# Optimization experiments

Measured on AMD Instinct MI355X. Metric: run time of the kernel, lower is better.

The kernel has to match this reference:

```python
import jax, jax.numpy as jnp
import numpy as np

DIM = 768
HEADS = 12
HEAD_DIM = DIM // HEADS
RANK = 8
SCALING = 1.0 / RANK  # lora_alpha / r
SCALE = HEAD_DIM ** -0.5


def setup_inputs() -> dict:
    key = jax.random.key(0)
    ks = jax.random.split(key, 14)
    B, N, D, r = 4, 1024, DIM, RANK
    s = lambda k, shape, sd=0.02: jax.random.normal(k, shape, jnp.float32) * sd
    return {
        "x": jax.random.normal(ks[0], (B, N, D), jnp.float32),
        "qkv_w": s(ks[1], (3 * D, D)),
        "qkv_b": s(ks[2], (3 * D,)),
        "q_base_w": s(ks[3], (D, D)),
        "q_base_b": s(ks[4], (D,)),
        "q_A": s(ks[5], (r, D), 1.0 / r),
        "q_B": s(ks[6], (D, r)),
        "k_base_w": s(ks[7], (D, D)),
        "k_base_b": s(ks[8], (D,)),
        "k_A": s(ks[9], (r, D), 1.0 / r),
        "k_B": s(ks[10], (D, r)),
        "proj_w": s(ks[11], (D, D)),
        "proj_b": s(ks[12], (D,)),
    }


def _lora_linear(x, w, b, A, Bm):
    # base linear + LoRA delta: x@w.T + b + (x@A.T)@B.T * scaling
    return x @ w.T + b + ((x @ A.T) @ Bm.T) * SCALING


def reference(x, qkv_w, qkv_b, q_base_w, q_base_b, q_A, q_B,
              k_base_w, k_base_b, k_A, k_B, proj_w, proj_b):
    B, N, D = x.shape
    H, hd = HEADS, HEAD_DIM
    qkv = (x @ qkv_w.T + qkv_b).reshape(B, N, 3, H, hd).transpose(2, 0, 3, 1, 4)
    q, k, v = qkv[0], qkv[1], qkv[2]  # [B,H,N,hd]
    q_delta = _lora_linear(x, q_base_w, q_base_b, q_A, q_B).reshape(B, N, H, hd).transpose(0, 2, 1, 3)
    k_delta = _lora_linear(x, k_base_w, k_base_b, k_A, k_B).reshape(B, N, H, hd).transpose(0, 2, 1, 3)
    q = q + q_delta
    k = k + k_delta
    attn = jnp.einsum('bhnd,bhmd->bhnm', q, k) * SCALE
    attn = jax.nn.softmax(attn, axis=-1)
    out = jnp.einsum('bhnm,bhmd->bhnd', attn, v)
    out = out.transpose(0, 2, 1, 3).reshape(B, N, D)
    return out @ proj_w.T + proj_b
```

## Files before the change

### kernel.cpp

```cpp
#include <hip/hip_runtime.h>
#include <hip/hip_bf16.h>


typedef _Float16 half8 __attribute__((ext_vector_type(8)));
typedef float f32x4 __attribute__((ext_vector_type(4)));

typedef __attribute__((address_space(3))) unsigned int lds_u32;
typedef __attribute__((address_space(1))) const unsigned int glob_u32;

__device__ __forceinline__ void glds16(const void* g, void* l) {
    __builtin_amdgcn_global_load_lds((glob_u32*)g, (lds_u32*)l, 16, 0, 0);
}

__device__ __forceinline__ float pk2f16(float a, float b) {
    return __builtin_bit_cast(float, __builtin_amdgcn_cvt_pkrtz(a, b));
}

#define SMSCALE 0.18033688011112042f

constexpr size_t OFF_WX = 0;
constexpr size_t OFF_PH = OFF_WX + (size_t)2304*800*2;
constexpr size_t OFF_XE = OFF_PH + (size_t)768*768*2;
constexpr size_t OFF_QH = OFF_XE + (size_t)4096*800*2;
constexpr size_t OFF_KH = OFF_QH + (size_t)48*1024*64*2;
constexpr size_t OFF_VT = OFF_KH + (size_t)48*1024*64*2;
constexpr size_t OFF_AO = OFF_VT + (size_t)48*1024*64*2;

__global__ __launch_bounds__(256)
void prep(const float* __restrict__ qkv_w, const float* __restrict__ qkv_b,
          const float* __restrict__ qw, const float* __restrict__ qbias,
          const float* __restrict__ kw, const float* __restrict__ kbias,
          const float* __restrict__ proj_w, const float* __restrict__ qB,
          const float* __restrict__ kB,
          _Float16* __restrict__ Wx, _Float16* __restrict__ Ph) {
    const int t = threadIdx.x, bb = blockIdx.x;
    if (bb < 2304) {
        const int n = bb;
        const float rs = (n < 768) ? SMSCALE : 1.0f;
        const float* wsrc = qkv_w + (size_t)n * 768;
        const float* fold = (n < 768) ? (qw + (size_t)n * 768)
                          : (n < 1536 ? (kw + (size_t)(n - 768) * 768) : nullptr);
        _Float16* dst = Wx + (size_t)n * 800;
#pragma unroll
        for (int i = 0; i < 3; ++i) {
            const int c = t + i * 256;
            float v = wsrc[c];
            if (fold) v += fold[c];
            dst[c] = (_Float16)(v * rs);
        }
        if (t < 32) {
            float v = 0.f;
            if (t < 8)       { if (n < 768) v = rs * 0.125f * qB[n * 8 + t]; }
            else if (t < 16) { if (n >= 768 && n < 1536) v = 0.125f * kB[(size_t)(n - 768) * 8 + (t - 8)]; }
            else if (t == 16) v = rs * (qkv_b[n] + (n < 768 ? qbias[n] : (n < 1536 ? kbias[n - 768] : 0.f)));
            dst[768 + t] = (_Float16)v;
        }
    } else {
        const size_t idx = ((size_t)(bb - 2304) * 256 + t) * 4;
        const float4 v = *(const float4*)(proj_w + idx);
        _Float16* d = Ph + idx;
        d[0] = (_Float16)v.x; d[1] = (_Float16)v.y;
        d[2] = (_Float16)v.z; d[3] = (_Float16)v.w;
    }
}

__global__ __launch_bounds__(256)
void lora_xa(const float* __restrict__ x, const float* __restrict__ qA,
             const float* __restrict__ kA, _Float16* __restrict__ Xe) {
    __shared__ float As_[16][772];
    __shared__ float xs[8][768];
    const int t = threadIdx.x, m0 = blockIdx.x * 8;

#pragma unroll
    for (int i = t * 4; i < 12288; i += 1024) {
        const int r = i / 768, c = i - r * 768;
        const float4 v = *(const float4*)((r < 8 ? qA + (size_t)r * 768 : kA + (size_t)(r - 8) * 768) + c);
        As_[r][c] = v.x; As_[r][c + 1] = v.y; As_[r][c + 2] = v.z; As_[r][c + 3] = v.w;
    }
#pragma unroll
    for (int i = t * 4; i < 6144; i += 1024) {
        const int r = i / 768, c = i - r * 768;
        const float4 v = *(const float4*)(x + (size_t)(m0 + r) * 768 + c);
        xs[r][c] = v.x; xs[r][c + 1] = v.y; xs[r][c + 2] = v.z; xs[r][c + 3] = v.w;
        _Float16* d = Xe + (size_t)(m0 + r) * 800 + c;
        d[0] = (_Float16)v.x; d[1] = (_Float16)v.y; d[2] = (_Float16)v.z; d[3] = (_Float16)v.w;
    }
    __syncthreads();

    const int j = t >> 4, lane = t & 15;
#pragma unroll
    for (int r = 0; r < 8; ++r) {
        float acc = 0.f;
        for (int k = lane; k < 768; k += 16) acc += xs[r][k] * As_[j][k];
        acc += __shfl_xor(acc, 1); acc += __shfl_xor(acc, 2);
        acc += __shfl_xor(acc, 4); acc += __shfl_xor(acc, 8);
        if (lane == 0) Xe[(size_t)(m0 + r) * 800 + 768 + j] = (_Float16)acc;
    }
    if (t < 128) {
        const int r = t >> 4, c = t & 15;
        Xe[(size_t)(m0 + r) * 800 + 784 + c] = (c == 0) ? (_Float16)1.f : (_Float16)0.f;
    }
}

template<int BM, int BN, int MODE>
__global__ __launch_bounds__(256)
void gemm_h(const _Float16* __restrict__ A, const _Float16* __restrict__ Bw,
            const int lda, const int ldb, const int nsteps,
            const float* __restrict__ bias,
            _Float16* __restrict__ Oq, _Float16* __restrict__ Ok, _Float16* __restrict__ Ov,
            float* __restrict__ Co) {
    constexpr int CA = BM / 16, CB = BN / 16, CT = CA + CB;
    constexpr int MI = BM / 32, NI = BN / 32;
    __shared__ __align__(16) _Float16 As[2][BM * 32];
    __shared__ __align__(16) _Float16 Bs[2][BN * 32];
    const int t = threadIdx.x;
    const int w = t >> 6, l = t & 63;
    const int l15 = l & 15, lg = l >> 4;
    const int wm = w >> 1, wn = w & 1;

    const int gx = gridDim.x;
    int lin = blockIdx.y * gx + blockIdx.x;
    lin = (lin & 7) * ((gx * gridDim.y) >> 3) + (lin >> 3);
    const int n0 = (lin % gx) * BN, m0 = (lin / gx) * BM;

    const _Float16* Abase = A + (size_t)(m0 + l15) * lda + lg * 8;
    const _Float16* Bbase = Bw + (size_t)(n0 + l15) * ldb + lg * 8;

    f32x4 acc[MI][NI];
#pragma unroll
    for (int mi = 0; mi < MI; ++mi)
#pragma unroll
        for (int ni = 0; ni < NI; ++ni) acc[mi][ni] = 0.f;

#pragma unroll
    for (int c = w; c < CT; c += 4) {
        if (c < CA) glds16(Abase + (size_t)(c * 16) * lda, &As[0][c * 512]);
        else        glds16(Bbase + (size_t)((c - CA) * 16) * ldb, &Bs[0][(c - CA) * 512]);
    }
    __syncthreads();

    for (int s = 0; s < nsteps; ++s) {
        const int cur = s & 1;
        if (s + 1 < nsteps) {
            const int ko = (s + 1) * 32;
#pragma unroll
            for (int c = w; c < CT; c += 4) {
                if (c < CA) glds16(Abase + (size_t)(c * 16) * lda + ko, &As[cur ^ 1][c * 512]);
                else        glds16(Bbase + (size_t)((c - CA) * 16) * ldb + ko, &Bs[cur ^ 1][(c - CA) * 512]);
            }
        }
        half8 a[MI], b[NI];
#pragma unroll
        for (int mi = 0; mi < MI; ++mi) a[mi] = *(const half8*)&As[cur][(wm * MI + mi) * 512 + l * 8];
#pragma unroll
        for (int ni = 0; ni < NI; ++ni) b[ni] = *(const half8*)&Bs[cur][(wn * NI + ni) * 512 + l * 8];
#pragma unroll
        for (int mi = 0; mi < MI; ++mi)
#pragma unroll
            for (int ni = 0; ni < NI; ++ni)
                acc[mi][ni] = __builtin_amdgcn_mfma_f32_16x16x32_f16(a[mi], b[ni], acc[mi][ni], 0, 0, 0);
        __syncthreads();
    }

    if (MODE == 0) {
        const int sel = (n0 >= 1536) ? 2 : (n0 >= 768 ? 1 : 0);
        const int b_ = m0 >> 10, nnb = m0 & 1023;
        if (sel < 2) {
            _Float16* dst = (sel == 0) ? Oq : Ok;
            const int jb = n0 - sel * 768;
#pragma unroll
            for (int mi = 0; mi < MI; ++mi)
#pragma unroll
                for (int reg = 0; reg < 4; ++reg) {
                    const int nn = nnb + wm * (BM / 2) + mi * 16 + lg * 4 + reg;
#pragma unroll
                    for (int ni = 0; ni < NI; ++ni) {
                        const int jj = jb + wn * (BN / 2) + ni * 16 + l15;
                        const int h = jj >> 6, d = jj & 63;
                        dst[(((size_t)(b_ * 12 + h)) * 1024 + nn) * 64 + d] = (_Float16)acc[mi][ni][reg];
                    }
                }
        } else {
#pragma unroll
            for (int mi = 0; mi < MI; ++mi) {
                const int nn = nnb + wm * (BM / 2) + mi * 16 + lg * 4;
#pragma unroll
                for (int ni = 0; ni < NI; ++ni) {
                    const int jj = (n0 - 1536) + wn * (BN / 2) + ni * 16 + l15;
                    const int h = jj >> 6, d = jj & 63;
                    float2 pv;
                    pv.x = pk2f16(acc[mi][ni][0], acc[mi][ni][1]);
                    pv.y = pk2f16(acc[mi][ni][2], acc[mi][ni][3]);
                    *(float2*)&Ov[(((size_t)(b_ * 12 + h)) * 64 + d) * 1024 + nn] = pv;
                }
            }
        }
    } else {
#pragma unroll
        for (int mi = 0; mi < MI; ++mi)
#pragma unroll
            for (int reg = 0; reg < 4; ++reg) {
                const int m = m0 + wm * (BM / 2) + mi * 16 + lg * 4 + reg;
#pragma unroll
                for (int ni = 0; ni < NI; ++ni) {
                    const int n = n0 + wn * (BN / 2) + ni * 16 + l15;
                    Co[(size_t)m * 768 + n] = acc[mi][ni][reg] + bias[n];
                }
            }
    }
}

#define STAGEK(kbt, buf) { \
_Pragma("unroll") \
    for (int i = 0; i < 4; ++i) { \
        const int c = w * 4 + i; \
        glds16(Kp + (size_t)((kbt) * 64 + (c >> 1) * 16 + l15) * 64 + (c & 1) * 32 + lg * 8, &Ks[buf][c * 512]); \
    } }
#define STAGEV(kbt, buf) { \
_Pragma("unroll") \
    for (int i = 0; i < 4; ++i) { \
        const int c = w * 4 + i; \
        glds16(Vp + (size_t)((c >> 1) * 16 + l15) * 1024 + (kbt) * 64 + (c & 1) * 32 + lg * 8, &Vs[buf][c * 512]); \
    } }
#define QK(buf, s) { \
    half8 kreg[8]; \
_Pragma("unroll") \
    for (int c = 0; c < 8; ++c) kreg[c] = *(const half8*)&Ks[buf][c * 512 + l * 8]; \
_Pragma("unroll") \
    for (int mi = 0; mi < 2; ++mi) \
_Pragma("unroll") \
        for (int nj = 0; nj < 4; ++nj) { \
            s[mi][nj] = 0.f; \
_Pragma("unroll") \
            for (int kh = 0; kh < 2; ++kh) \
                s[mi][nj] = __builtin_amdgcn_mfma_f32_16x16x32_f16(kreg[nj * 2 + kh], qf[mi][kh], s[mi][nj], 0, 0, 0); \
        } }
#define EXPP(ph, s) { \
_Pragma("unroll") \
    for (int mi = 0; mi < 2; ++mi) { \
        float ls = 0.f; \
_Pragma("unroll") \
        for (int nj = 0; nj < 4; ++nj) { \
            const float p0 = __builtin_amdgcn_exp2f(s[mi][nj][0]); \
            const float p1 = __builtin_amdgcn_exp2f(s[mi][nj][1]); \
            const float p2 = __builtin_amdgcn_exp2f(s[mi][nj][2]); \
            const float p3 = __builtin_amdgcn_exp2f(s[mi][nj][3]); \
            ls += (p0 + p1) + (p2 + p3); \
            float2 pk; \
            pk.x = pk2f16(p0, p1); \
            pk.y = pk2f16(p2, p3); \
            const int off = (mi * 2 + (nj >> 1)) * 512 + (2 * (nj & 1) + (lg >> 1)) * 128 \
                          + l15 * 8 + 4 * (lg & 1); \
            *(float2*)&Ps[w][ph][off] = pk; \
        } \
        lsum[mi] += ls; \
    } }
#define PV(ph, buf) { \
    half8 pf[2][2]; \
_Pragma("unroll") \
    for (int mi = 0; mi < 2; ++mi) \
_Pragma("unroll") \
        for (int kh = 0; kh < 2; ++kh) \
            pf[mi][kh] = *(const half8*)&Ps[w][ph][(mi * 2 + kh) * 512 + l * 8]; \
_Pragma("unroll") \
    for (int fj = 0; fj < 4; ++fj) \
_Pragma("unroll") \
        for (int kh = 0; kh < 2; ++kh) { \
            const half8 vf = *(const half8*)&Vs[buf][(fj * 2 + kh) * 512 + l * 8]; \
_Pragma("unroll") \
            for (int mi = 0; mi < 2; ++mi) \
                o[mi][fj] = __builtin_amdgcn_mfma_f32_16x16x32_f16(pf[mi][kh], vf, o[mi][fj], 0, 0, 0); \
        } }

__global__ __launch_bounds__(128)
void attn5(const _Float16* __restrict__ Q, const _Float16* __restrict__ K,
           const _Float16* __restrict__ Vt, _Float16* __restrict__ AO) {
    __shared__ __align__(16) _Float16 Ks[2][4096];
    __shared__ __align__(16) _Float16 Vs[2][4096];
    __shared__ __align__(16) _Float16 Ps[2][2][2048];
    __shared__ float sums[2][32];
    const int t = threadIdx.x;
    const int w = t >> 6, l = t & 63;
    const int l15 = l & 15, lg = l >> 4;

    int lin = blockIdx.y * 16 + blockIdx.x;
    lin = (lin & 7) * 96 + (lin >> 3);
    const int qb = lin & 15, bh = lin >> 4;

    const _Float16* Qp = Q  + (size_t)bh * 65536;
    const _Float16* Kp = K  + (size_t)bh * 65536;
    const _Float16* Vp = Vt + (size_t)bh * 65536;

    STAGEK(0, 0); STAGEK(1, 1); STAGEV(0, 0);
    half8 qf[2][2];
#pragma unroll
    for (int mi = 0; mi < 2; ++mi)
#pragma unroll
        for (int kh = 0; kh < 2; ++kh)
            qf[mi][kh] = *(const half8*)&Qp[(size_t)(qb * 64 + w * 32 + mi * 16 + l15) * 64 + kh * 32 + lg * 8];

    f32x4 o[2][4];
#pragma unroll
    for (int mi = 0; mi < 2; ++mi)
#pragma unroll
        for (int fj = 0; fj < 4; ++fj) o[mi][fj] = 0.f;
    float lsum[2] = {0.f, 0.f};
    __syncthreads();

    {
        f32x4 s[2][4];
        QK(0, s);
        EXPP(0, s);
    }
    __syncthreads();

    for (int kb = 0; kb < 15; ++kb) {
        const int cb = kb & 1, nb = cb ^ 1;
        if (kb + 2 < 16) STAGEK(kb + 2, cb);
        STAGEV(kb + 1, nb);
        f32x4 s[2][4];
        __builtin_amdgcn_s_setprio(1);
        QK(nb, s);
        PV(cb, cb);
        __builtin_amdgcn_s_setprio(0);
        EXPP(nb, s);
        __syncthreads();
    }
    PV(1, 1);

#pragma unroll
    for (int mi = 0; mi < 2; ++mi) {
        float tot = lsum[mi];
        tot += __shfl_xor(tot, 16);
        tot += __shfl_xor(tot, 32);
        if (lg == 0) sums[w][mi * 16 + l15] = tot;
    }
    __builtin_amdgcn_wave_barrier();

    const int b_ = bh / 12, h = bh % 12;
#pragma unroll
    for (int mi = 0; mi < 2; ++mi)
#pragma unroll
        for (int reg = 0; reg < 4; ++reg) {
            const float inv = 1.f / sums[w][mi * 16 + lg * 4 + reg];
            const int tok = qb * 64 + w * 32 + mi * 16 + lg * 4 + reg;
            const size_t base = ((size_t)(b_ * 1024 + tok)) * 768 + h * 64;
#pragma unroll
            for (int fj = 0; fj < 4; ++fj)
                AO[base + fj * 16 + l15] = (_Float16)(o[mi][fj][reg] * inv);
        }
}

extern "C" void kernel_launch(void* const* d_in, const int* in_sizes, int n_in,
                              void* d_out, int out_size, void* d_ws, size_t ws_size,
                              hipStream_t stream) {
    (void)in_sizes; (void)n_in; (void)out_size; (void)ws_size;
    const float* x      = (const float*)d_in[0];
    const float* qkv_w  = (const float*)d_in[1];
    const float* qkv_b  = (const float*)d_in[2];
    const float* q_bw   = (const float*)d_in[3];
    const float* q_bb   = (const float*)d_in[4];
    const float* q_A    = (const float*)d_in[5];
    const float* q_B    = (const float*)d_in[6];
    const float* k_bw   = (const float*)d_in[7];
    const float* k_bb   = (const float*)d_in[8];
    const float* k_A    = (const float*)d_in[9];
    const float* k_B    = (const float*)d_in[10];
    const float* proj_w = (const float*)d_in[11];
    const float* proj_b = (const float*)d_in[12];
    float* out = (float*)d_out;
    char*  ws  = (char*)d_ws;

    _Float16* Wx = (_Float16*)(ws + OFF_WX);
    _Float16* Ph = (_Float16*)(ws + OFF_PH);
    _Float16* Xe = (_Float16*)(ws + OFF_XE);
    _Float16* Qh = (_Float16*)(ws + OFF_QH);
    _Float16* Kh = (_Float16*)(ws + OFF_KH);
    _Float16* Vt = (_Float16*)(ws + OFF_VT);
    _Float16* AO = (_Float16*)(ws + OFF_AO);

    prep<<<dim3(2880), dim3(256), 0, stream>>>(qkv_w, qkv_b, q_bw, q_bb, k_bw, k_bb,
                                               proj_w, q_B, k_B, Wx, Ph);
    lora_xa<<<dim3(512), dim3(256), 0, stream>>>(x, q_A, k_A, Xe);
    gemm_h<128, 96, 0><<<dim3(24, 32), dim3(256), 0, stream>>>(
        Xe, Wx, 800, 800, 25, nullptr, Qh, Kh, Vt, nullptr);
    attn5<<<dim3(16, 48), dim3(128), 0, stream>>>(Qh, Kh, Vt, AO);
    gemm_h<64, 96, 1><<<dim3(8, 64), dim3(256), 0, stream>>>(
        AO, Ph, 768, 768, 24, proj_b, nullptr, nullptr, nullptr, out);
}
```

Measured before the change: 110.9 us.

## Load V tiles directly into registers instead of staging through LDS

```diff
diff --git a/kernel.cpp b/kernel.cpp
--- a/kernel.cpp
+++ b/kernel.cpp
@@ -216,12 +216,10 @@
         const int c = w * 4 + i; \
         glds16(Kp + (size_t)((kbt) * 64 + (c >> 1) * 16 + l15) * 64 + (c & 1) * 32 + lg * 8, &Ks[buf][c * 512]); \
     } }
-#define STAGEV(kbt, buf) { \
-_Pragma("unroll") \
-    for (int i = 0; i < 4; ++i) { \
-        const int c = w * 4 + i; \
-        glds16(Vp + (size_t)((c >> 1) * 16 + l15) * 1024 + (kbt) * 64 + (c & 1) * 32 + lg * 8, &Vs[buf][c * 512]); \
-    } }
+#define LOADVG(dst, kbt) { \
+_Pragma("unroll") \
+    for (int c = 0; c < 8; ++c) \
+        dst[c] = *(const half8*)(Vp + (size_t)((c >> 1) * 16 + l15) * 1024 + (kbt) * 64 + (c & 1) * 32 + lg * 8); }
 #define QK(buf, s) { \
     half8 kreg[8]; \
 _Pragma("unroll") \
@@ -255,7 +253,7 @@
         } \
         lsum[mi] += ls; \
     } }
-#define PV(ph, buf) { \
+#define PVR(ph, vreg) { \
     half8 pf[2][2]; \
 _Pragma("unroll") \
     for (int mi = 0; mi < 2; ++mi) \
@@ -265,18 +263,15 @@
 _Pragma("unroll") \
     for (int fj = 0; fj < 4; ++fj) \
 _Pragma("unroll") \
-        for (int kh = 0; kh < 2; ++kh) { \
-            const half8 vf = *(const half8*)&Vs[buf][(fj * 2 + kh) * 512 + l * 8]; \
+        for (int kh = 0; kh < 2; ++kh) \
 _Pragma("unroll") \
             for (int mi = 0; mi < 2; ++mi) \
-                o[mi][fj] = __builtin_amdgcn_mfma_f32_16x16x32_f16(pf[mi][kh], vf, o[mi][fj], 0, 0, 0); \
-        } }
-
-__global__ __launch_bounds__(128)
-void attn5(const _Float16* __restrict__ Q, const _Float16* __restrict__ K,
+                o[mi][fj] = __builtin_amdgcn_mfma_f32_16x16x32_f16(pf[mi][kh], vreg[fj * 2 + kh], o[mi][fj], 0, 0, 0); }
+
+__global__ __launch_bounds__(128, 2)
+void attn6(const _Float16* __restrict__ Q, const _Float16* __restrict__ K,
            const _Float16* __restrict__ Vt, _Float16* __restrict__ AO) {
     __shared__ __align__(16) _Float16 Ks[2][4096];
-    __shared__ __align__(16) _Float16 Vs[2][4096];
     __shared__ __align__(16) _Float16 Ps[2][2][2048];
     __shared__ float sums[2][32];
     const int t = threadIdx.x;
@@ -291,7 +286,9 @@
     const _Float16* Kp = K  + (size_t)bh * 65536;
     const _Float16* Vp = Vt + (size_t)bh * 65536;
 
-    STAGEK(0, 0); STAGEK(1, 1); STAGEV(0, 0);
+    STAGEK(0, 0); STAGEK(1, 1);
+    half8 va[8], vb[8];
+    LOADVG(va, 0);
     half8 qf[2][2];
 #pragma unroll
     for (int mi = 0; mi < 2; ++mi)
@@ -314,19 +311,39 @@
     }
     __syncthreads();
 
-    for (int kb = 0; kb < 15; ++kb) {
-        const int cb = kb & 1, nb = cb ^ 1;
-        if (kb + 2 < 16) STAGEK(kb + 2, cb);
-        STAGEV(kb + 1, nb);
+    for (int it = 0; it < 7; ++it) {
+        const int kb = 2 * it;
+        {
+            STAGEK(kb + 2, 0);
+            LOADVG(vb, kb + 1);
+            f32x4 s[2][4];
+            __builtin_amdgcn_s_setprio(1);
+            QK(1, s);
+            PVR(0, va);
+            __builtin_amdgcn_s_setprio(0);
+            EXPP(1, s);
+            __syncthreads();
+        }
+        {
+            STAGEK(kb + 3, 1);
+            LOADVG(va, kb + 2);
+            f32x4 s[2][4];
+            __builtin_amdgcn_s_setprio(1);
+            QK(0, s);
+            PVR(1, vb);
+            __builtin_amdgcn_s_setprio(0);
+            EXPP(0, s);
+            __syncthreads();
+        }
+    }
+    {
+        LOADVG(vb, 15);
         f32x4 s[2][4];
-        __builtin_amdgcn_s_setprio(1);
-        QK(nb, s);
-        PV(cb, cb);
-        __builtin_amdgcn_s_setprio(0);
-        EXPP(nb, s);
-        __syncthreads();
-    }
-    PV(1, 1);
+        QK(1, s);
+        PVR(0, va);
+        EXPP(1, s);
+    }
+    PVR(1, vb);
 
 #pragma unroll
     for (int mi = 0; mi < 2; ++mi) {
@@ -384,7 +401,7 @@
     lora_xa<<<dim3(512), dim3(256), 0, stream>>>(x, q_A, k_A, Xe);
     gemm_h<128, 96, 0><<<dim3(24, 32), dim3(256), 0, stream>>>(
         Xe, Wx, 800, 800, 25, nullptr, Qh, Kh, Vt, nullptr);
-    attn5<<<dim3(16, 48), dim3(128), 0, stream>>>(Qh, Kh, Vt, AO);
+    attn6<<<dim3(16, 48), dim3(128), 0, stream>>>(Qh, Kh, Vt, AO);
     gemm_h<64, 96, 1><<<dim3(8, 64), dim3(256), 0, stream>>>(
         AO, Ph, 768, 768, 24, proj_b, nullptr, nullptr, nullptr, out);
 }
```

New measurement: 118.6 us. +7.0%, slower.
